# Kernel optimization log

Hardware: AMD Instinct MI355X
Metric: run time of the kernel (lower is better)

Reference implementation:

```python
import jax, jax.numpy as jnp
import numpy as np

N_NODES = 100000
N_EDGES = 1600000
D_IN, D_HID, D_OUT = 128, 128, 64


def gcn_conv(x, src, dst, deg_inv_sqrt, W, b, n_nodes):
    # PyG GCNConv (normalize=True, add_self_loops already folded into src/dst/deg):
    # out = scatter_add( d^{-1/2}[src] * d^{-1/2}[dst] * (x @ W)[src] ) + b
    h = x @ W                                    # [N, d_out]
    norm = deg_inv_sqrt[src] * deg_inv_sqrt[dst]  # [E+N]
    msg = h[src] * norm[:, None]                  # [E+N, d_out] (edge gather)
    out = jax.ops.segment_sum(msg, dst, num_segments=n_nodes)
    return out + b


def _augment(edge_index, n_nodes):
    # add self-loops and compute symmetric-normalization degrees (in-degree at dst)
    loop = jnp.arange(n_nodes, dtype=edge_index.dtype)
    src = jnp.concatenate([edge_index[0], loop])
    dst = jnp.concatenate([edge_index[1], loop])
    deg = jax.ops.segment_sum(jnp.ones_like(dst, dtype=jnp.float32), dst,
                              num_segments=n_nodes)
    deg_inv_sqrt = jnp.where(deg > 0, jax.lax.rsqrt(jnp.maximum(deg, 1.0)), 0.0)
    return src, dst, deg_inv_sqrt


def setup_inputs() -> dict:
    key = jax.random.key(0)
    k1, k2, k3, k4 = jax.random.split(key, 4)
    x = jax.random.normal(k1, (N_NODES, D_IN), dtype=jnp.float32)
    edge_index = jax.random.randint(k2, (2, N_EDGES), 0, N_NODES, dtype=jnp.int32)
    s = 1.0 / np.sqrt(D_IN)
    W1 = jax.random.uniform(k3, (D_IN, D_HID), dtype=jnp.float32, minval=-s, maxval=s)
    b1 = jnp.zeros((D_HID,), dtype=jnp.float32)
    s2 = 1.0 / np.sqrt(D_HID)
    W2 = jax.random.uniform(k4, (D_HID, D_OUT), dtype=jnp.float32, minval=-s2, maxval=s2)
    b2 = jnp.zeros((D_OUT,), dtype=jnp.float32)
    return {"x": x, "edge_index": edge_index, "W1": W1, "b1": b1, "W2": W2, "b2": b2}


def reference(x, edge_index, W1, b1, W2, b2):
    n_nodes = x.shape[0]
    src, dst, dinv = _augment(edge_index, n_nodes)
    h = gcn_conv(x, src, dst, dinv, W1, b1, n_nodes)
    h = jax.nn.relu(h)
    # dropout is identity in eval mode (F.dropout with training=False)
    out = gcn_conv(h, src, dst, dinv, W2, b2, n_nodes)
    return out
```

## Files before the change

### kernel.cpp

```cpp
#include <hip/hip_runtime.h>

typedef unsigned int uint;
typedef unsigned short ushort;
typedef __attribute__((ext_vector_type(8))) short short8v;
typedef __attribute__((ext_vector_type(4))) float f32x4;

#define NBMAX 512
#define BSHIFT 8

__device__ __forceinline__ ushort f2bf(float f) {
    uint u = __float_as_uint(f);
    u += 0x7fffu + ((u >> 16) & 1u);
    return (ushort)(u >> 16);
}
__device__ __forceinline__ float bf2f(ushort h) {
    return __uint_as_float(((uint)h) << 16);
}


__global__ void bucket_hist(const int* __restrict__ dst, int* __restrict__ bcnt,
                            int E, int nbk) {
    __shared__ int s[NBMAX];
    int t = threadIdx.x;
    for (int i = t; i < nbk; i += 256) s[i] = 0;
    __syncthreads();
    int i0 = blockIdx.x * 4096 + t;
#pragma unroll
    for (int k = 0; k < 16; ++k) {
        int i = i0 + k * 256;
        if (i < E) atomicAdd(&s[dst[i] >> BSHIFT], 1);
    }
    __syncthreads();
    for (int i = t; i < nbk; i += 256) if (s[i] > 0) atomicAdd(&bcnt[i], s[i]);
}

__global__ void bucket_scan(const int* __restrict__ bcnt, int* __restrict__ bstart,
                            int* __restrict__ bcur, int nbk) {
    __shared__ int s[512];
    int t = threadIdx.x;
    int v = (t < nbk) ? bcnt[t] : 0;
    s[t] = v;
    __syncthreads();
    for (int o = 1; o < 512; o <<= 1) {
        int tv = (t >= o) ? s[t - o] : 0;
        __syncthreads();
        s[t] += tv;
        __syncthreads();
    }
    if (t < nbk) {
        int ex = s[t] - v;
        bstart[t] = ex;
        bcur[t] = ex;
    }
}

__global__ void bucket_scatter(const int* __restrict__ src, const int* __restrict__ dst,
                               int* __restrict__ bcur, int* __restrict__ tsw, int E) {
    __shared__ int cnt[NBMAX];
    __shared__ int base[NBMAX];
    int t = threadIdx.x;
    for (int i = t; i < NBMAX; i += 256) cnt[i] = 0;
    __syncthreads();
    int i0 = blockIdx.x * 4096 + t;
    int p_[16], b_[16], r_[16];
#pragma unroll
    for (int k = 0; k < 16; ++k) {
        int i = i0 + k * 256;
        if (i < E) {
            int s = src[i], d = dst[i];
            int bb = d >> BSHIFT;
            b_[k] = bb;
            p_[k] = s | ((d & ((1 << BSHIFT) - 1)) << 17);
            r_[k] = atomicAdd(&cnt[bb], 1);
        } else {
            b_[k] = -1;
        }
    }
    __syncthreads();
    for (int i = t; i < NBMAX; i += 256) if (cnt[i] > 0) base[i] = atomicAdd(&bcur[i], cnt[i]);
    __syncthreads();
#pragma unroll
    for (int k = 0; k < 16; ++k) {
        if (b_[k] >= 0) {
            int p = base[b_[k]] + r_[k];
            tsw[p] = p_[k];
        }
    }
}

__global__ void sort_bucket(const int* __restrict__ tsw, const int* __restrict__ bstart,
                            float* __restrict__ dinv, int* __restrict__ rp,
                            int* __restrict__ edata, int N, int E, int nbk) {
    __shared__ int cnt[256];
    __shared__ int cursor[256];
    int b = blockIdx.x;
    int t = threadIdx.x;
    int estart = bstart[b];
    int eend = (b + 1 < nbk) ? bstart[b + 1] : E;

    cnt[t] = 0;
    __syncthreads();
    for (int i = estart + t; i < eend; i += 256) {
        atomicAdd(&cnt[(uint)tsw[i] >> 17], 1);
    }
    __syncthreads();

    int node = (b << BSHIFT) + t;
    int self = (node < N) ? 1 : 0;
    int deg = cnt[t];
    int v = deg + self;
    cursor[t] = v;
    __syncthreads();
    for (int o = 1; o < 256; o <<= 1) {
        int tv = (t >= o) ? cursor[t - o] : 0;
        __syncthreads();
        cursor[t] += tv;
        __syncthreads();
    }
    int ex = cursor[t] - v;
    int gbase = estart + (b << BSHIFT);

    if (node < N) {
        dinv[node] = rsqrtf((float)(deg + 1));
        rp[node] = gbase + ex;
        edata[gbase + ex] = node;
    }
    if (b == nbk - 1 && t == 0) rp[N] = E + N;
    cursor[t] = ex + self;
    __syncthreads();

    for (int i = estart + t; i < eend; i += 256) {
        uint rec = (uint)tsw[i];
        int pos = gbase + atomicAdd(&cursor[rec >> 17], 1);
        edata[pos] = (int)(rec & 0x1FFFFu);
    }
}


__global__ void prep_w(const float* __restrict__ W1, const float* __restrict__ W2,
                       ushort* __restrict__ Wt1s, ushort* __restrict__ Wt2s) {
    int t = blockIdx.x * 256 + threadIdx.x;
    int total = gridDim.x * 256;
    for (int idx = t; idx < 128 * 128; idx += total) {
        int nn = idx >> 7, kk = idx & 127;
        uint byte = (uint)nn * 256u + (uint)kk * 2u;
        byte ^= (uint)((nn & 7) << 4);
        Wt1s[byte >> 1] = f2bf(W1[kk * 128 + nn]);
    }
    for (int idx = t; idx < 64 * 128; idx += total) {
        int nn = idx >> 7, kk = idx & 127;
        uint byte = (uint)nn * 256u + (uint)kk * 2u;
        byte ^= (uint)((nn & 7) << 4);
        Wt2s[byte >> 1] = f2bf(W2[kk * 64 + nn]);
    }
}


template <int NCOLS, bool IN_BF16>
__launch_bounds__(256)
__global__ void gemm_mfma(const void* __restrict__ Xv, const ushort* __restrict__ Wimg,
                          ushort* __restrict__ H, int n) {
    constexpr int NT = NCOLS / 16;
    __shared__ ushort sW[NCOLS * 128];
    {
        const uint4* src = (const uint4*)Wimg;
        uint4* dst = (uint4*)sW;
        constexpr int NV = NCOLS * 128 * 2 / 16;
        for (int i = threadIdx.x; i < NV; i += 256) dst[i] = src[i];
    }
    __syncthreads();

    const int w  = threadIdx.x >> 6;
    const int l  = threadIdx.x & 63;
    const int lm = l & 15, lk = l >> 4;
    const int row_base = blockIdx.x * 128 + w * 32;

    f32x4 acc[2][NT];
#pragma unroll
    for (int mt = 0; mt < 2; ++mt)
#pragma unroll
        for (int nt = 0; nt < NT; ++nt) {
            f32x4 z = {0.f, 0.f, 0.f, 0.f};
            acc[mt][nt] = z;
        }

    int r0 = row_base + lm;
    int r1 = row_base + 16 + lm;
    int r0c = r0 < n ? r0 : n - 1;
    int r1c = r1 < n ? r1 : n - 1;

#pragma unroll
    for (int kb = 0; kb < 4; ++kb) {
        short8v a0, a1;
        if constexpr (IN_BF16) {
            const ushort* X = (const ushort*)Xv;
            a0 = *(const short8v*)(X + (size_t)r0c * 128 + kb * 32 + lk * 8);
            a1 = *(const short8v*)(X + (size_t)r1c * 128 + kb * 32 + lk * 8);
        } else {
            const float* X = (const float*)Xv;
            const float* p0 = X + (size_t)r0c * 128 + kb * 32 + lk * 8;
            const float* p1 = X + (size_t)r1c * 128 + kb * 32 + lk * 8;
            float4 u0 = *(const float4*)p0;
            float4 v0 = *(const float4*)(p0 + 4);
            float4 u1 = *(const float4*)p1;
            float4 v1 = *(const float4*)(p1 + 4);
            a0[0] = (short)f2bf(u0.x); a0[1] = (short)f2bf(u0.y);
            a0[2] = (short)f2bf(u0.z); a0[3] = (short)f2bf(u0.w);
            a0[4] = (short)f2bf(v0.x); a0[5] = (short)f2bf(v0.y);
            a0[6] = (short)f2bf(v0.z); a0[7] = (short)f2bf(v0.w);
            a1[0] = (short)f2bf(u1.x); a1[1] = (short)f2bf(u1.y);
            a1[2] = (short)f2bf(u1.z); a1[3] = (short)f2bf(u1.w);
            a1[4] = (short)f2bf(v1.x); a1[5] = (short)f2bf(v1.y);
            a1[6] = (short)f2bf(v1.z); a1[7] = (short)f2bf(v1.w);
        }
#pragma unroll
        for (int nt = 0; nt < NT; ++nt) {
            int nn = nt * 16 + lm;
            uint byte = (uint)nn * 256u + (uint)kb * 64u + (uint)lk * 16u;
            byte ^= (uint)((nn & 7) << 4);
            short8v b = *(const short8v*)((const char*)sW + byte);
            acc[0][nt] = __builtin_amdgcn_mfma_f32_16x16x32_bf16(a0, b, acc[0][nt], 0, 0, 0);
            acc[1][nt] = __builtin_amdgcn_mfma_f32_16x16x32_bf16(a1, b, acc[1][nt], 0, 0, 0);
        }
    }

#pragma unroll
    for (int mt = 0; mt < 2; ++mt)
#pragma unroll
        for (int nt = 0; nt < NT; ++nt)
#pragma unroll
            for (int r = 0; r < 4; ++r) {
                int row = row_base + mt * 16 + lk * 4 + r;
                if (row < n) H[(size_t)row * NCOLS + nt * 16 + lm] = f2bf(acc[mt][nt][r]);
            }
}


template <bool RELU>
__launch_bounds__(256)
__global__ void agg128(const ushort* __restrict__ H, const int* __restrict__ rp,
                       const int* __restrict__ edata, const float* __restrict__ dinv,
                       const float* __restrict__ bias, ushort* __restrict__ out, int n) {
    int gw = (blockIdx.x * 256 + threadIdx.x) >> 6;
    int lane = threadIdx.x & 63;
    if (gw >= n) return;
    const int h = lane >> 5, c = lane & 31;
    int e = rp[gw], end = rp[gw + 1];
    const float dg = dinv[gw];
    float a0 = 0.f, a1 = 0.f, a2 = 0.f, a3 = 0.f;

    for (; e < end; e += 16) {
        int rem = end - e;
        int s = 0;
        float wl = 0.f;
        if (lane < rem && lane < 16) {
            s = edata[e + lane];
            wl = dinv[s];
        }
#pragma unroll
        for (int j = 0; j < 8; ++j) {
            int   si = __shfl(s, 2 * j + h);
            float w  = __shfl(wl, 2 * j + h) * dg;
            uint2 hv = *(const uint2*)&H[(size_t)si * 128 + c * 4];
            a0 += w * bf2f((ushort)hv.x); a1 += w * bf2f((ushort)(hv.x >> 16));
            a2 += w * bf2f((ushort)hv.y); a3 += w * bf2f((ushort)(hv.y >> 16));
        }
    }
    a0 += __shfl_xor(a0, 32); a1 += __shfl_xor(a1, 32);
    a2 += __shfl_xor(a2, 32); a3 += __shfl_xor(a3, 32);
    if (h == 0) {
        a0 += bias[c * 4 + 0]; a1 += bias[c * 4 + 1];
        a2 += bias[c * 4 + 2]; a3 += bias[c * 4 + 3];
        if (RELU) {
            a0 = fmaxf(a0, 0.f); a1 = fmaxf(a1, 0.f);
            a2 = fmaxf(a2, 0.f); a3 = fmaxf(a3, 0.f);
        }
        uint2 pk;
        pk.x = (uint)f2bf(a0) | ((uint)f2bf(a1) << 16);
        pk.y = (uint)f2bf(a2) | ((uint)f2bf(a3) << 16);
        *(uint2*)&out[(size_t)gw * 128 + c * 4] = pk;
    }
}

__launch_bounds__(256)
__global__ void agg64(const ushort* __restrict__ H, const int* __restrict__ rp,
                      const int* __restrict__ edata, const float* __restrict__ dinv,
                      const float* __restrict__ bias, float* __restrict__ out, int n) {
    int gw = (blockIdx.x * 256 + threadIdx.x) >> 6;
    int lane = threadIdx.x & 63;
    if (gw >= n) return;
    const int q = lane >> 4, c = lane & 15;
    int e = rp[gw], end = rp[gw + 1];
    const float dg = dinv[gw];
    float a0 = 0.f, a1 = 0.f, a2 = 0.f, a3 = 0.f;

    for (; e < end; e += 16) {
        int rem = end - e;
        int s = 0;
        float wl = 0.f;
        if (lane < rem && lane < 16) {
            s = edata[e + lane];
            wl = dinv[s];
        }
#pragma unroll
        for (int j = 0; j < 4; ++j) {
            int   si = __shfl(s, 4 * j + q);
            float w  = __shfl(wl, 4 * j + q) * dg;
            uint2 hv = *(const uint2*)&H[(size_t)si * 64 + c * 4];
            a0 += w * bf2f((ushort)hv.x); a1 += w * bf2f((ushort)(hv.x >> 16));
            a2 += w * bf2f((ushort)hv.y); a3 += w * bf2f((ushort)(hv.y >> 16));
        }
    }
    a0 += __shfl_xor(a0, 16); a0 += __shfl_xor(a0, 32);
    a1 += __shfl_xor(a1, 16); a1 += __shfl_xor(a1, 32);
    a2 += __shfl_xor(a2, 16); a2 += __shfl_xor(a2, 32);
    a3 += __shfl_xor(a3, 16); a3 += __shfl_xor(a3, 32);
    if (q == 0) {
        a0 += bias[c * 4 + 0]; a1 += bias[c * 4 + 1];
        a2 += bias[c * 4 + 2]; a3 += bias[c * 4 + 3];
        *(float4*)&out[(size_t)gw * 64 + c * 4] = make_float4(a0, a1, a2, a3);
    }
}

__global__ void zero_out(float* __restrict__ out, int n) {
    int i = blockIdx.x * 256 + threadIdx.x;
    if (i < n) out[i] = 0.f;
}


extern "C" void kernel_launch(void* const* d_in, const int* in_sizes, int n_in,
                              void* d_out, int out_size, void* d_ws, size_t ws_size,
                              hipStream_t stream) {
    const float* x  = (const float*)d_in[0];
    const int*   ei = (const int*)d_in[1];
    const float* W1 = (const float*)d_in[2];
    const float* b1 = (const float*)d_in[3];
    const float* W2 = (const float*)d_in[4];
    const float* b2 = (const float*)d_in[5];
    float* out = (float*)d_out;

    const int N = in_sizes[0] / 128;
    const int E = in_sizes[1] / 2;
    const int* srcp = ei;
    const int* dstp = ei + E;

    char* base = (char*)d_ws;
    size_t off = 0;
    auto alloc = [&](size_t bytes) -> void* {
        void* p = base + off;
        off += (bytes + 15) & ~(size_t)15;
        return p;
    };
    ushort* H1    = (ushort*)alloc((size_t)N * 128 * 2);
    ushort* A1    = (ushort*)alloc((size_t)N * 128 * 2);
    ushort* Wt1s  = (ushort*)alloc(128 * 128 * 2);
    ushort* Wt2s  = (ushort*)alloc(64 * 128 * 2);
    float*  dinv  = (float*)alloc((size_t)N * 4);
    int*    rp    = (int*)alloc((size_t)(N + 1) * 4);
    int*    bcnt  = (int*)alloc(NBMAX * 4);
    int*    bstart= (int*)alloc(NBMAX * 4);
    int*    bcur  = (int*)alloc(NBMAX * 4);
    int*    edata = (int*)alloc((size_t)(E + N) * 4);
    ushort* H2    = H1;

    int* tsw = (int*)A1;

    int nbk = (N + (1 << BSHIFT) - 1) >> BSHIFT;
    if (off > ws_size || (size_t)E * 4 > (size_t)N * 256 || N > (1 << 17) || nbk > NBMAX) {
        zero_out<<<(out_size + 255) / 256, 256, 0, stream>>>(out, out_size);
        return;
    }
    int nchunk = (E + 4095) / 4096;

    hipMemsetAsync(bcnt, 0, NBMAX * sizeof(int), stream);
    bucket_hist<<<nchunk, 256, 0, stream>>>(dstp, bcnt, E, nbk);
    bucket_scan<<<1, 512, 0, stream>>>(bcnt, bstart, bcur, nbk);
    bucket_scatter<<<nchunk, 256, 0, stream>>>(srcp, dstp, bcur, tsw, E);
    sort_bucket<<<nbk, 256, 0, stream>>>(tsw, bstart, dinv, rp, edata, N, E, nbk);
    prep_w<<<32, 256, 0, stream>>>(W1, W2, Wt1s, Wt2s);

    gemm_mfma<128, false><<<(N + 127) / 128, 256, 0, stream>>>(x, Wt1s, H1, N);
    agg128<true><<<(N + 3) / 4, 256, 0, stream>>>(H1, rp, edata, dinv, b1, A1, N);
    gemm_mfma<64, true><<<(N + 127) / 128, 256, 0, stream>>>(A1, Wt2s, H2, N);
    agg64<<<(N + 3) / 4, 256, 0, stream>>>(H2, rp, edata, dinv, b2, out, N);
}
```

Baseline: 212.1 us.

## Split features into 32-column slabs and pre-scale rows by dinv in GEMM

The GEMM output is stored as column slabs of 32 bf16 values per node, and each row is pre-multiplied by the source degree normalization. Aggregation then runs one block group per slab, so each gathered row is a 64-byte segment and the per-edge dinv lookup and multiply disappear; the destination dinv is applied once at the end. Padding edges point to a zeroed sentinel row instead of being masked by weight. Block-index interleaving across slabs is meant to keep each slab's gather working set cache-resident, at the cost of reading edge lists once per slab.

```diff
diff --git a/kernel.cpp b/kernel.cpp
--- a/kernel.cpp
+++ b/kernel.cpp
@@ -12,9 +12,6 @@
     uint u = __float_as_uint(f);
     u += 0x7fffu + ((u >> 16) & 1u);
     return (ushort)(u >> 16);
-}
-__device__ __forceinline__ float bf2f(ushort h) {
-    return __uint_as_float(((uint)h) << 16);
 }
 
 
@@ -136,6 +133,11 @@
     }
 }
 
+__global__ void zero_rows(ushort* __restrict__ Hz, int strideH) {
+    int i = threadIdx.x;
+    if (i < 128) Hz[(size_t)(i >> 5) * strideH + (i & 31)] = 0;
+}
+
 
 __global__ void prep_w(const float* __restrict__ W1, const float* __restrict__ W2,
                        ushort* __restrict__ Wt1s, ushort* __restrict__ Wt2s) {
@@ -159,7 +161,8 @@
 template <int NCOLS, bool IN_BF16>
 __launch_bounds__(256)
 __global__ void gemm_mfma(const void* __restrict__ Xv, const ushort* __restrict__ Wimg,
-                          ushort* __restrict__ H, int n) {
+                          ushort* __restrict__ H, const float* __restrict__ dinv,
+                          int n, int strideA, int strideH) {
     constexpr int NT = NCOLS / 16;
     __shared__ ushort sW[NCOLS * 128];
     {
@@ -194,8 +197,8 @@
         short8v a0, a1;
         if constexpr (IN_BF16) {
             const ushort* X = (const ushort*)Xv;
-            a0 = *(const short8v*)(X + (size_t)r0c * 128 + kb * 32 + lk * 8);
-            a1 = *(const short8v*)(X + (size_t)r1c * 128 + kb * 32 + lk * 8);
+            a0 = *(const short8v*)(X + (size_t)kb * strideA + (size_t)r0c * 32 + lk * 8);
+            a1 = *(const short8v*)(X + (size_t)kb * strideA + (size_t)r1c * 32 + lk * 8);
         } else {
             const float* X = (const float*)Xv;
             const float* p0 = X + (size_t)r0c * 128 + kb * 32 + lk * 8;
@@ -224,6 +227,14 @@
         }
     }
 
+    float dvs[2][4];
+#pragma unroll
+    for (int mt = 0; mt < 2; ++mt)
+#pragma unroll
+        for (int r = 0; r < 4; ++r) {
+            int row = row_base + mt * 16 + lk * 4 + r;
+            dvs[mt][r] = (row < n) ? dinv[row] : 0.f;
+        }
 #pragma unroll
     for (int mt = 0; mt < 2; ++mt)
 #pragma unroll
@@ -231,94 +242,74 @@
 #pragma unroll
             for (int r = 0; r < 4; ++r) {
                 int row = row_base + mt * 16 + lk * 4 + r;
-                if (row < n) H[(size_t)row * NCOLS + nt * 16 + lm] = f2bf(acc[mt][nt][r]);
+                if (row < n) {
+                    size_t off = (size_t)(nt >> 1) * strideH + (size_t)row * 32 + (nt & 1) * 16 + lm;
+                    H[off] = f2bf(acc[mt][nt][r] * dvs[mt][r]);
+                }
             }
 }
 
 
-template <bool RELU>
+template <bool RELU, bool OUT_BF16>
 __launch_bounds__(256)
-__global__ void agg128(const ushort* __restrict__ H, const int* __restrict__ rp,
-                       const int* __restrict__ edata, const float* __restrict__ dinv,
-                       const float* __restrict__ bias, ushort* __restrict__ out, int n) {
-    int gw = (blockIdx.x * 256 + threadIdx.x) >> 6;
+__global__ void agg_slab(const ushort* __restrict__ H, const int* __restrict__ rp,
+                         const int* __restrict__ edata, const float* __restrict__ dinv,
+                         const float* __restrict__ bias, void* __restrict__ outv,
+                         int N, int G, int strideH, int strideO, int slabdiv) {
+    int bid = blockIdx.x;
+    int oct = bid & 7;
+    int slab = oct >> slabdiv;
+    int per = (1 << slabdiv);
+    int g = (bid >> 3) * per + (oct & (per - 1));
+    if (g >= G) return;
+    int node = g * 4 + (threadIdx.x >> 6);
+    if (node >= N) return;
     int lane = threadIdx.x & 63;
-    if (gw >= n) return;
-    const int h = lane >> 5, c = lane & 31;
-    int e = rp[gw], end = rp[gw + 1];
-    const float dg = dinv[gw];
+    const int gi = lane >> 3, c = lane & 7;
+    const ushort* Hs = H + (size_t)slab * strideH;
+
+    int e = rp[node], end = rp[node + 1];
     float a0 = 0.f, a1 = 0.f, a2 = 0.f, a3 = 0.f;
 
     for (; e < end; e += 16) {
         int rem = end - e;
-        int s = 0;
-        float wl = 0.f;
-        if (lane < rem && lane < 16) {
-            s = edata[e + lane];
-            wl = dinv[s];
-        }
-#pragma unroll
-        for (int j = 0; j < 8; ++j) {
-            int   si = __shfl(s, 2 * j + h);
-            float w  = __shfl(wl, 2 * j + h) * dg;
-            uint2 hv = *(const uint2*)&H[(size_t)si * 128 + c * 4];
-            a0 += w * bf2f((ushort)hv.x); a1 += w * bf2f((ushort)(hv.x >> 16));
-            a2 += w * bf2f((ushort)hv.y); a3 += w * bf2f((ushort)(hv.y >> 16));
-        }
-    }
-    a0 += __shfl_xor(a0, 32); a1 += __shfl_xor(a1, 32);
-    a2 += __shfl_xor(a2, 32); a3 += __shfl_xor(a3, 32);
-    if (h == 0) {
-        a0 += bias[c * 4 + 0]; a1 += bias[c * 4 + 1];
-        a2 += bias[c * 4 + 2]; a3 += bias[c * 4 + 3];
+        int md = N;
+        if (lane < 16 && lane < rem) md = edata[e + lane];
+#pragma unroll
+        for (int j = 0; j < 2; ++j) {
+            int si = __shfl(md, j * 8 + gi);
+            uint2 hv = *(const uint2*)(Hs + (size_t)si * 32 + c * 4);
+            a0 += __uint_as_float(hv.x << 16);
+            a1 += __uint_as_float(hv.x & 0xffff0000u);
+            a2 += __uint_as_float(hv.y << 16);
+            a3 += __uint_as_float(hv.y & 0xffff0000u);
+        }
+    }
+    a0 += __shfl_xor(a0, 8); a0 += __shfl_xor(a0, 16); a0 += __shfl_xor(a0, 32);
+    a1 += __shfl_xor(a1, 8); a1 += __shfl_xor(a1, 16); a1 += __shfl_xor(a1, 32);
+    a2 += __shfl_xor(a2, 8); a2 += __shfl_xor(a2, 16); a2 += __shfl_xor(a2, 32);
+    a3 += __shfl_xor(a3, 8); a3 += __shfl_xor(a3, 16); a3 += __shfl_xor(a3, 32);
+
+    if (lane < 8) {
+        float dg = dinv[node];
+        float4 bv = *(const float4*)&bias[slab * 32 + lane * 4];
+        a0 = dg * a0 + bv.x; a1 = dg * a1 + bv.y;
+        a2 = dg * a2 + bv.z; a3 = dg * a3 + bv.w;
         if (RELU) {
             a0 = fmaxf(a0, 0.f); a1 = fmaxf(a1, 0.f);
             a2 = fmaxf(a2, 0.f); a3 = fmaxf(a3, 0.f);
         }
-        uint2 pk;
-        pk.x = (uint)f2bf(a0) | ((uint)f2bf(a1) << 16);
-        pk.y = (uint)f2bf(a2) | ((uint)f2bf(a3) << 16);
-        *(uint2*)&out[(size_t)gw * 128 + c * 4] = pk;
-    }
-}
-
-__launch_bounds__(256)
-__global__ void agg64(const ushort* __restrict__ H, const int* __restrict__ rp,
-                      const int* __restrict__ edata, const float* __restrict__ dinv,
-                      const float* __restrict__ bias, float* __restrict__ out, int n) {
-    int gw = (blockIdx.x * 256 + threadIdx.x) >> 6;
-    int lane = threadIdx.x & 63;
-    if (gw >= n) return;
-    const int q = lane >> 4, c = lane & 15;
-    int e = rp[gw], end = rp[gw + 1];
-    const float dg = dinv[gw];
-    float a0 = 0.f, a1 = 0.f, a2 = 0.f, a3 = 0.f;
-
-    for (; e < end; e += 16) {
-        int rem = end - e;
-        int s = 0;
-        float wl = 0.f;
-        if (lane < rem && lane < 16) {
-            s = edata[e + lane];
-            wl = dinv[s];
-        }
-#pragma unroll
-        for (int j = 0; j < 4; ++j) {
-            int   si = __shfl(s, 4 * j + q);
-            float w  = __shfl(wl, 4 * j + q) * dg;
-            uint2 hv = *(const uint2*)&H[(size_t)si * 64 + c * 4];
-            a0 += w * bf2f((ushort)hv.x); a1 += w * bf2f((ushort)(hv.x >> 16));
-            a2 += w * bf2f((ushort)hv.y); a3 += w * bf2f((ushort)(hv.y >> 16));
-        }
-    }
-    a0 += __shfl_xor(a0, 16); a0 += __shfl_xor(a0, 32);
-    a1 += __shfl_xor(a1, 16); a1 += __shfl_xor(a1, 32);
-    a2 += __shfl_xor(a2, 16); a2 += __shfl_xor(a2, 32);
-    a3 += __shfl_xor(a3, 16); a3 += __shfl_xor(a3, 32);
-    if (q == 0) {
-        a0 += bias[c * 4 + 0]; a1 += bias[c * 4 + 1];
-        a2 += bias[c * 4 + 2]; a3 += bias[c * 4 + 3];
-        *(float4*)&out[(size_t)gw * 64 + c * 4] = make_float4(a0, a1, a2, a3);
+        if (OUT_BF16) {
+            ushort* out = (ushort*)outv;
+            uint2 pk;
+            pk.x = (uint)f2bf(a0) | ((uint)f2bf(a1) << 16);
+            pk.y = (uint)f2bf(a2) | ((uint)f2bf(a3) << 16);
+            *(uint2*)(out + (size_t)slab * strideO + (size_t)node * 32 + lane * 4) = pk;
+        } else {
+            float* out = (float*)outv;
+            *(float4*)(out + (size_t)node * 64 + slab * 32 + lane * 4) =
+                make_float4(a0, a1, a2, a3);
+        }
     }
 }
 
@@ -351,7 +342,7 @@
         off += (bytes + 15) & ~(size_t)15;
         return p;
     };
-    ushort* H1    = (ushort*)alloc((size_t)N * 128 * 2);
+    ushort* H1    = (ushort*)alloc((size_t)(N + 1) * 128 * 2);
     ushort* A1    = (ushort*)alloc((size_t)N * 128 * 2);
     ushort* Wt1s  = (ushort*)alloc(128 * 128 * 2);
     ushort* Wt2s  = (ushort*)alloc(64 * 128 * 2);
@@ -365,6 +356,9 @@
 
     int* tsw = (int*)A1;
 
+    const int strideH = (N + 1) * 32;
+    const int strideA = N * 32;
+
     int nbk = (N + (1 << BSHIFT) - 1) >> BSHIFT;
     if (off > ws_size || (size_t)E * 4 > (size_t)N * 256 || N > (1 << 17) || nbk > NBMAX) {
         zero_out<<<(out_size + 255) / 256, 256, 0, stream>>>(out, out_size);
@@ -377,10 +371,14 @@
     bucket_scan<<<1, 512, 0, stream>>>(bcnt, bstart, bcur, nbk);
     bucket_scatter<<<nchunk, 256, 0, stream>>>(srcp, dstp, bcur, tsw, E);
     sort_bucket<<<nbk, 256, 0, stream>>>(tsw, bstart, dinv, rp, edata, N, E, nbk);
+    zero_rows<<<1, 128, 0, stream>>>(H1 + (size_t)N * 32, strideH);
     prep_w<<<32, 256, 0, stream>>>(W1, W2, Wt1s, Wt2s);
 
-    gemm_mfma<128, false><<<(N + 127) / 128, 256, 0, stream>>>(x, Wt1s, H1, N);
-    agg128<true><<<(N + 3) / 4, 256, 0, stream>>>(H1, rp, edata, dinv, b1, A1, N);
-    gemm_mfma<64, true><<<(N + 127) / 128, 256, 0, stream>>>(A1, Wt2s, H2, N);
-    agg64<<<(N + 3) / 4, 256, 0, stream>>>(H2, rp, edata, dinv, b2, out, N);
-}
+    int G = (N + 3) / 4;
+    gemm_mfma<128, false><<<(N + 127) / 128, 256, 0, stream>>>(x, Wt1s, H1, dinv, N, 0, strideH);
+    agg_slab<true, true><<<8 * ((G + 1) / 2), 256, 0, stream>>>(
+        H1, rp, edata, dinv, b1, A1, N, G, strideH, strideA, 1);
+    gemm_mfma<64, true><<<(N + 127) / 128, 256, 0, stream>>>(A1, Wt2s, H2, dinv, N, strideA, strideH);
+    agg_slab<false, false><<<8 * ((G + 3) / 4), 256, 0, stream>>>(
+        H2, rp, edata, dinv, b2, out, N, G, strideH, 0, 2);
+}
```

New measurement: 316.0 us. 1.49x slower.

## Fold source-node normalization into GEMM epilogue and pad gathers with zero row

Applied to the files above, without the earlier changes.

The GEMM epilogue now scales each output row by dinv[row], so the aggregation kernels no longer gather dinv[src] per edge. The per-edge multiply becomes a plain add, and the destination dinv and bias are applied once per node after the reduction. The aggregation loop now handles 32 edges per iteration, with out-of-range slots pointing at an extra zero row (index N) that replaces the per-lane masking. This removes a dependent random load per edge and some multiplies, at the cost of rounding the pre-scaled values to bf16 and issuing two extra tiny launches.

```diff
diff --git a/kernel.cpp b/kernel.cpp
--- a/kernel.cpp
+++ b/kernel.cpp
@@ -12,9 +12,6 @@
     uint u = __float_as_uint(f);
     u += 0x7fffu + ((u >> 16) & 1u);
     return (ushort)(u >> 16);
-}
-__device__ __forceinline__ float bf2f(ushort h) {
-    return __uint_as_float(((uint)h) << 16);
 }
 
 
@@ -136,6 +133,11 @@
     }
 }
 
+__global__ void zero_row(ushort* __restrict__ Hz, int len) {
+    int i = threadIdx.x;
+    if (i < len) Hz[i] = 0;
+}
+
 
 __global__ void prep_w(const float* __restrict__ W1, const float* __restrict__ W2,
                        ushort* __restrict__ Wt1s, ushort* __restrict__ Wt2s) {
@@ -159,7 +161,7 @@
 template <int NCOLS, bool IN_BF16>
 __launch_bounds__(256)
 __global__ void gemm_mfma(const void* __restrict__ Xv, const ushort* __restrict__ Wimg,
-                          ushort* __restrict__ H, int n) {
+                          ushort* __restrict__ H, const float* __restrict__ dinv, int n) {
     constexpr int NT = NCOLS / 16;
     __shared__ ushort sW[NCOLS * 128];
     {
@@ -224,6 +226,14 @@
         }
     }
 
+    float dvs[2][4];
+#pragma unroll
+    for (int mt = 0; mt < 2; ++mt)
+#pragma unroll
+        for (int r = 0; r < 4; ++r) {
+            int row = row_base + mt * 16 + lk * 4 + r;
+            dvs[mt][r] = (row < n) ? dinv[row] : 0.f;
+        }
 #pragma unroll
     for (int mt = 0; mt < 2; ++mt)
 #pragma unroll
@@ -231,7 +241,7 @@
 #pragma unroll
             for (int r = 0; r < 4; ++r) {
                 int row = row_base + mt * 16 + lk * 4 + r;
-                if (row < n) H[(size_t)row * NCOLS + nt * 16 + lm] = f2bf(acc[mt][nt][r]);
+                if (row < n) H[(size_t)row * NCOLS + nt * 16 + lm] = f2bf(acc[mt][nt][r] * dvs[mt][r]);
             }
 }
 
@@ -240,37 +250,34 @@
 __launch_bounds__(256)
 __global__ void agg128(const ushort* __restrict__ H, const int* __restrict__ rp,
                        const int* __restrict__ edata, const float* __restrict__ dinv,
-                       const float* __restrict__ bias, ushort* __restrict__ out, int n) {
+                       const float* __restrict__ bias, ushort* __restrict__ out, int N) {
     int gw = (blockIdx.x * 256 + threadIdx.x) >> 6;
     int lane = threadIdx.x & 63;
-    if (gw >= n) return;
+    if (gw >= N) return;
     const int h = lane >> 5, c = lane & 31;
     int e = rp[gw], end = rp[gw + 1];
-    const float dg = dinv[gw];
     float a0 = 0.f, a1 = 0.f, a2 = 0.f, a3 = 0.f;
 
-    for (; e < end; e += 16) {
-        int rem = end - e;
-        int s = 0;
-        float wl = 0.f;
-        if (lane < rem && lane < 16) {
-            s = edata[e + lane];
-            wl = dinv[s];
-        }
-#pragma unroll
-        for (int j = 0; j < 8; ++j) {
-            int   si = __shfl(s, 2 * j + h);
-            float w  = __shfl(wl, 2 * j + h) * dg;
+    for (; e < end; e += 32) {
+        int md = N;
+        if (lane < 32 && e + lane < end) md = edata[e + lane];
+#pragma unroll
+        for (int j = 0; j < 16; ++j) {
+            int si = __shfl(md, 2 * j + h);
             uint2 hv = *(const uint2*)&H[(size_t)si * 128 + c * 4];
-            a0 += w * bf2f((ushort)hv.x); a1 += w * bf2f((ushort)(hv.x >> 16));
-            a2 += w * bf2f((ushort)hv.y); a3 += w * bf2f((ushort)(hv.y >> 16));
+            a0 += __uint_as_float(hv.x << 16);
+            a1 += __uint_as_float(hv.x & 0xffff0000u);
+            a2 += __uint_as_float(hv.y << 16);
+            a3 += __uint_as_float(hv.y & 0xffff0000u);
         }
     }
     a0 += __shfl_xor(a0, 32); a1 += __shfl_xor(a1, 32);
     a2 += __shfl_xor(a2, 32); a3 += __shfl_xor(a3, 32);
     if (h == 0) {
-        a0 += bias[c * 4 + 0]; a1 += bias[c * 4 + 1];
-        a2 += bias[c * 4 + 2]; a3 += bias[c * 4 + 3];
+        float dg = dinv[gw];
+        float4 bv = *(const float4*)&bias[c * 4];
+        a0 = dg * a0 + bv.x; a1 = dg * a1 + bv.y;
+        a2 = dg * a2 + bv.z; a3 = dg * a3 + bv.w;
         if (RELU) {
             a0 = fmaxf(a0, 0.f); a1 = fmaxf(a1, 0.f);
             a2 = fmaxf(a2, 0.f); a3 = fmaxf(a3, 0.f);
@@ -285,30 +292,25 @@
 __launch_bounds__(256)
 __global__ void agg64(const ushort* __restrict__ H, const int* __restrict__ rp,
                       const int* __restrict__ edata, const float* __restrict__ dinv,
-                      const float* __restrict__ bias, float* __restrict__ out, int n) {
+                      const float* __restrict__ bias, float* __restrict__ out, int N) {
     int gw = (blockIdx.x * 256 + threadIdx.x) >> 6;
     int lane = threadIdx.x & 63;
-    if (gw >= n) return;
+    if (gw >= N) return;
     const int q = lane >> 4, c = lane & 15;
     int e = rp[gw], end = rp[gw + 1];
-    const float dg = dinv[gw];
     float a0 = 0.f, a1 = 0.f, a2 = 0.f, a3 = 0.f;
 
-    for (; e < end; e += 16) {
-        int rem = end - e;
-        int s = 0;
-        float wl = 0.f;
-        if (lane < rem && lane < 16) {
-            s = edata[e + lane];
-            wl = dinv[s];
-        }
-#pragma unroll
-        for (int j = 0; j < 4; ++j) {
-            int   si = __shfl(s, 4 * j + q);
-            float w  = __shfl(wl, 4 * j + q) * dg;
+    for (; e < end; e += 32) {
+        int md = N;
+        if (lane < 32 && e + lane < end) md = edata[e + lane];
+#pragma unroll
+        for (int j = 0; j < 8; ++j) {
+            int si = __shfl(md, 4 * j + q);
             uint2 hv = *(const uint2*)&H[(size_t)si * 64 + c * 4];
-            a0 += w * bf2f((ushort)hv.x); a1 += w * bf2f((ushort)(hv.x >> 16));
-            a2 += w * bf2f((ushort)hv.y); a3 += w * bf2f((ushort)(hv.y >> 16));
+            a0 += __uint_as_float(hv.x << 16);
+            a1 += __uint_as_float(hv.x & 0xffff0000u);
+            a2 += __uint_as_float(hv.y << 16);
+            a3 += __uint_as_float(hv.y & 0xffff0000u);
         }
     }
     a0 += __shfl_xor(a0, 16); a0 += __shfl_xor(a0, 32);
@@ -316,8 +318,10 @@
     a2 += __shfl_xor(a2, 16); a2 += __shfl_xor(a2, 32);
     a3 += __shfl_xor(a3, 16); a3 += __shfl_xor(a3, 32);
     if (q == 0) {
-        a0 += bias[c * 4 + 0]; a1 += bias[c * 4 + 1];
-        a2 += bias[c * 4 + 2]; a3 += bias[c * 4 + 3];
+        float dg = dinv[gw];
+        float4 bv = *(const float4*)&bias[c * 4];
+        a0 = dg * a0 + bv.x; a1 = dg * a1 + bv.y;
+        a2 = dg * a2 + bv.z; a3 = dg * a3 + bv.w;
         *(float4*)&out[(size_t)gw * 64 + c * 4] = make_float4(a0, a1, a2, a3);
     }
 }
@@ -351,7 +355,7 @@
         off += (bytes + 15) & ~(size_t)15;
         return p;
     };
-    ushort* H1    = (ushort*)alloc((size_t)N * 128 * 2);
+    ushort* H1    = (ushort*)alloc((size_t)(N + 1) * 128 * 2);
     ushort* A1    = (ushort*)alloc((size_t)N * 128 * 2);
     ushort* Wt1s  = (ushort*)alloc(128 * 128 * 2);
     ushort* Wt2s  = (ushort*)alloc(64 * 128 * 2);
@@ -377,10 +381,12 @@
     bucket_scan<<<1, 512, 0, stream>>>(bcnt, bstart, bcur, nbk);
     bucket_scatter<<<nchunk, 256, 0, stream>>>(srcp, dstp, bcur, tsw, E);
     sort_bucket<<<nbk, 256, 0, stream>>>(tsw, bstart, dinv, rp, edata, N, E, nbk);
+    zero_row<<<1, 128, 0, stream>>>(H1 + (size_t)N * 128, 128);
     prep_w<<<32, 256, 0, stream>>>(W1, W2, Wt1s, Wt2s);
 
-    gemm_mfma<128, false><<<(N + 127) / 128, 256, 0, stream>>>(x, Wt1s, H1, N);
+    gemm_mfma<128, false><<<(N + 127) / 128, 256, 0, stream>>>(x, Wt1s, H1, dinv, N);
     agg128<true><<<(N + 3) / 4, 256, 0, stream>>>(H1, rp, edata, dinv, b1, A1, N);
-    gemm_mfma<64, true><<<(N + 127) / 128, 256, 0, stream>>>(A1, Wt2s, H2, N);
+    zero_row<<<1, 64, 0, stream>>>(H2 + (size_t)N * 64, 64);
+    gemm_mfma<64, true><<<(N + 127) / 128, 256, 0, stream>>>(A1, Wt2s, H2, dinv, N);
     agg64<<<(N + 3) / 4, 256, 0, stream>>>(H2, rp, edata, dinv, b2, out, N);
 }
```

Result: no change. 216.1 us (+1.9%).
